# Kernel optimization log

Hardware: AMD Instinct MI355X
Metric: run time of the kernel (lower is better)

The kernel has to match this reference:

```python
import jax, jax.numpy as jnp
import numpy as np

N_QUBITS = 8
N_LAYERS = 2


def _apply_1q(state, U, wire, n):
    # state: (bs, 2**n); U: (2,2) fixed or (bs,2,2) batched; wire 0 = most significant
    bs = state.shape[0]
    left = 2 ** wire
    right = 2 ** (n - wire - 1)
    s = state.reshape(bs, left, 2, right)
    if U.ndim == 2:
        s = jnp.einsum('ij,bljr->blir', U, s)
    else:
        s = jnp.einsum('bij,bljr->blir', U, s)
    return s.reshape(bs, -1)


def _apply_ctrl(state, U, control, target, n):
    # apply 2x2 U on `target` where `control` qubit is |1>
    bs = state.shape[0]
    left = 2 ** control
    right = 2 ** (n - control - 1)
    s = state.reshape(bs, left, 2, right)
    s0 = s[:, :, 0, :].reshape(bs, -1)
    s1 = s[:, :, 1, :].reshape(bs, -1)
    t = target if target < control else target - 1  # target index among remaining n-1 wires
    s1 = _apply_1q(s1, U, t, n - 1)
    s = jnp.stack([s0.reshape(bs, left, right), s1.reshape(bs, left, right)], axis=2)
    return s.reshape(bs, -1)


def _rz_batched(theta):
    h = 0.5 * theta
    c, s = jnp.cos(h), jnp.sin(h)
    z = jnp.zeros_like(c)
    row0 = jnp.stack([c - 1j * s, z + 0j], axis=-1)
    row1 = jnp.stack([z + 0j, c + 1j * s], axis=-1)
    return jnp.stack([row0, row1], axis=-2).astype(jnp.complex64)  # (bs,2,2)


def _ry_batched(theta):
    h = 0.5 * theta
    c, s = jnp.cos(h), jnp.sin(h)
    row0 = jnp.stack([c, -s], axis=-1)
    row1 = jnp.stack([s, c], axis=-1)
    return jnp.stack([row0, row1], axis=-2).astype(jnp.complex64)


def _rx_fixed(theta):
    h = 0.5 * theta
    c, s = jnp.cos(h), jnp.sin(h)
    return jnp.stack([jnp.stack([c + 0j, -1j * s]), jnp.stack([-1j * s, c + 0j])]).astype(jnp.complex64)


def _ry_fixed(theta):
    h = 0.5 * theta
    c, s = jnp.cos(h), jnp.sin(h)
    return jnp.stack([jnp.stack([c + 0j, -s + 0j]), jnp.stack([s + 0j, c + 0j])]).astype(jnp.complex64)


def _circuit(X, weights):
    bs, L = X.shape
    n = N_QUBITS
    vpq = L // n + 1  # var_per_qubit
    state = jnp.zeros((bs, 2 ** n), jnp.complex64).at[:, 0].set(1.0)
    H = jnp.asarray(np.array([[1, 1], [1, -1]], np.complex64) / np.sqrt(2))
    # encoding: Hadamard then alternating RZ/RY per qubit
    for q in range(n):
        state = _apply_1q(state, H, q, n)
        for i in range(vpq):
            idx = q * vpq + i
            if idx >= L:
                break
            th = X[:, idx]
            U = _rz_batched(th) if i % 2 == 0 else _ry_batched(th)
            state = _apply_1q(state, U, q, n)
    # entangling ring: layer 0 -> CRX, layer 1 -> CRY ((l+1)%2==0 -> CRY)
    for l in range(N_LAYERS):
        for i in range(n):
            th = weights[l, i]
            U = _ry_fixed(th) if (l + 1) % 2 == 0 else _rx_fixed(th)
            state = _apply_ctrl(state, U, i, (i + 1) % n, n)
    # PauliZ expectation on each wire
    p = state.real ** 2 + state.imag ** 2  # (bs, 256)
    outs = []
    for q in range(n):
        pq = p.reshape(bs, 2 ** q, 2, -1).sum(axis=(1, 3))  # (bs, 2)
        outs.append(pq[:, 0] - pq[:, 1])
    return jnp.stack(outs, axis=1)  # (bs, 8)


def setup_inputs() -> dict:
    key = jax.random.key(0)
    k1, k2 = jax.random.split(key)
    X = jax.random.normal(k1, (16384, 64), dtype=jnp.float32)
    weights = jax.random.normal(k2, (N_LAYERS, N_LAYERS * N_QUBITS), dtype=jnp.float32)
    return {"X": X, "weights": weights}


def reference(X, weights):
    return _circuit(X, weights)
```

## Files before the change

kernel.cpp:

```cpp
#include <hip/hip_runtime.h>

#define DEV __device__ __forceinline__
typedef float f32x2 __attribute__((ext_vector_type(2)));
typedef float f32x4 __attribute__((ext_vector_type(4)));

DEV float rdlane(float v, int l) {
  return __int_as_float(__builtin_amdgcn_readlane(__float_as_int(v), l));
}
DEV f32x2 pkfma(f32x2 a, f32x2 b, f32x2 c) { return __builtin_elementwise_fma(a, b, c); }
DEV f32x2 splat(float x) { return (f32x2){x, x}; }
DEV f32x2 swap2(f32x2 v) { return __builtin_shufflevector(v, v, 1, 0); }
DEV f32x2 cmul(f32x2 P, f32x2 F) {
  f32x2 t = swap2(P);
  f32x2 m = {-t.x, t.y};
  return pkfma(splat(F.y), m, splat(F.x) * P);
}

template <int CTRL>
DEV float dppmov(float v) {
  return __int_as_float(__builtin_amdgcn_update_dpp(
      0, __float_as_int(v), CTRL, 0xf, 0xf, true));
}
template <int M>
DEV float xorl(float v) {
  if constexpr (M == 1)       return dppmov<0xB1>(v);
  else if constexpr (M == 2)  return dppmov<0x4E>(v);
  else if constexpr (M == 8)  return dppmov<0x128>(v);
  else if constexpr (M == 4)
    return __int_as_float(__builtin_amdgcn_ds_swizzle(__float_as_int(v), 0x101F));
  else
    return __int_as_float(__builtin_amdgcn_ds_swizzle(__float_as_int(v), 0x401F));
}

template <int M, bool CRX, int R0, int RS>
DEV void gate_lane(f32x2 amp[8], int lane, float c1, float s1) {
  const f32x2 C2 = splat(c1);
  if constexpr (CRX) {
    const f32x2 S2 = {s1, -s1};
#pragma unroll
    for (int r = R0; r < 8; r += RS) {
      f32x2 p;
      p.x = xorl<M>(amp[r].y);
      p.y = xorl<M>(amp[r].x);
      amp[r] = pkfma(S2, p, C2 * amp[r]);
    }
  } else {
    const float sp = (lane & M) ? s1 : -s1;
    const f32x2 SP = splat(sp);
#pragma unroll
    for (int r = R0; r < 8; r += RS) {
      f32x2 p;
      p.x = xorl<M>(amp[r].x);
      p.y = xorl<M>(amp[r].y);
      amp[r] = pkfma(SP, p, C2 * amp[r]);
    }
  }
}

template <bool CRX>
DEV void gate_pair(f32x2& aI, f32x2& aJ, float c1, float s1) {
  const f32x2 C2 = splat(c1);
  f32x2 nI, nJ;
  if constexpr (CRX) {
    const f32x2 S2 = {s1, -s1};
    nI = pkfma(S2, swap2(aJ), C2 * aI);
    nJ = pkfma(S2, swap2(aI), C2 * aJ);
  } else {
    nI = pkfma(splat(-s1), aJ, C2 * aI);
    nJ = pkfma(splat(s1), aI, C2 * aJ);
  }
  aI = nI; aJ = nJ;
}

__global__ __launch_bounds__(256, 4) void qsim_kernel(const float* __restrict__ X,
                                                      const float* __restrict__ W,
                                                      float* __restrict__ out, int bs) {
  const int lane = threadIdx.x & 63;
  const int wave = blockIdx.x * (blockDim.x >> 6) + (threadIdx.x >> 6);
  const int b0 = wave * 2;
  if (b0 >= bs) return;

  const float w = W[(((lane & 15) >> 3) << 4) + (lane & 7)];

  const int ce = (lane >> 3) & 1;
  const int cq = lane & 7;
  int bb = b0 + ce; bb = bb >= bs ? bs - 1 : bb;
  const float* Xrow = X + (size_t)bb * 64;
  const int lb = (cq == 7) ? 55 : cq * 9;
  f32x4 v0, v1;
  __builtin_memcpy(&v0, Xrow + lb, 16);
  __builtin_memcpy(&v1, Xrow + lb + 4, 16);
  const float a8 = Xrow[lb + 8];
  float ang[9] = {v0.x, v0.y, v0.z, v0.w, v1.x, v1.y, v1.z, v1.w, a8};
  if (cq == 7) ang[0] = a8;

  const float Hc = 0.70710678118654752440f;
  f32x2 A = {Hc, 0.f}, B = {Hc, 0.f};
#pragma unroll
  for (int i = 0; i < 9; ++i) {
    float s, c;
    __sincosf(0.5f * ang[i], &s, &c);
    if (i > 0) {
      bool dead = (cq == 7);
      c = dead ? 1.f : c;
      s = dead ? 0.f : s;
    }
    if ((i & 1) == 0) {
      f32x2 nA = pkfma((f32x2){s, -s}, swap2(A), splat(c) * A);
      f32x2 nB = pkfma((f32x2){-s, s}, swap2(B), splat(c) * B);
      A = nA; B = nB;
    } else {
      f32x2 nA = pkfma(splat(-s), B, splat(c) * A);
      f32x2 nB = pkfma(splat(c), B, splat(s) * A);
      A = nA; B = nB;
    }
  }

  __shared__ f32x4 ldsAB[4][16];
  const int wvid = (threadIdx.x >> 6) & 3;
  if (lane < 16) ldsAB[wvid][lane] = (f32x4){A.x, A.y, B.x, B.y};
  __builtin_amdgcn_wave_barrier();

  float sw, cw;
  __sincosf(0.5f * w, &sw, &cw);

  const int half = lane >> 5;
  const int base = half * 8;
  const f32x2* b2 = (const f32x2*)&ldsAB[wvid][0];
  f32x2 P = b2[(base + 0) * 2 + ((lane >> 4) & 1)];
#pragma unroll
  for (int q = 1; q <= 4; ++q)
    P = cmul(P, b2[(base + q) * 2 + ((lane >> (4 - q)) & 1)]);
  f32x4 F5 = ldsAB[wvid][base + 5];
  f32x4 F6 = ldsAB[wvid][base + 6];
  f32x4 F7 = ldsAB[wvid][base + 7];
  f32x2 A5 = {F5.x, F5.y}, B5 = {F5.z, F5.w};
  f32x2 A6 = {F6.x, F6.y}, B6 = {F6.z, F6.w};
  f32x2 A7 = {F7.x, F7.y}, B7 = {F7.z, F7.w};
  f32x2 amp[8];
  {
    f32x2 t0 = cmul(P, A5), t1 = cmul(P, B5);
    f32x2 u00 = cmul(t0, A6), u01 = cmul(t0, B6);
    amp[0] = cmul(u00, A7); amp[1] = cmul(u00, B7);
    amp[2] = cmul(u01, A7); amp[3] = cmul(u01, B7);
    f32x2 u10 = cmul(t1, A6), u11 = cmul(t1, B6);
    amp[4] = cmul(u10, A7); amp[5] = cmul(u10, B7);
    amp[6] = cmul(u11, A7); amp[7] = cmul(u11, B7);
  }

#pragma unroll
  for (int l = 0; l < 2; ++l) {
    const bool isCRX = (l == 0);
#define CS(G, CBIT) \
    const float cg = rdlane(cw, G), sg = rdlane(sw, G); \
    const bool act = (lane >> (CBIT)) & 1; \
    const float c1 = act ? cg : 1.f, s1 = act ? sg : 0.f;
    { CS(l * 8 + 0, 4)
      if (isCRX) gate_lane<8, true, 0, 1>(amp, lane, c1, s1);
      else       gate_lane<8, false, 0, 1>(amp, lane, c1, s1); }
    { CS(l * 8 + 1, 3)
      if (isCRX) gate_lane<4, true, 0, 1>(amp, lane, c1, s1);
      else       gate_lane<4, false, 0, 1>(amp, lane, c1, s1); }
    { CS(l * 8 + 2, 2)
      if (isCRX) gate_lane<2, true, 0, 1>(amp, lane, c1, s1);
      else       gate_lane<2, false, 0, 1>(amp, lane, c1, s1); }
    { CS(l * 8 + 3, 1)
      if (isCRX) gate_lane<1, true, 0, 1>(amp, lane, c1, s1);
      else       gate_lane<1, false, 0, 1>(amp, lane, c1, s1); }
    { CS(l * 8 + 4, 0)
#pragma unroll
      for (int r = 0; r < 4; ++r) {
        if (isCRX) gate_pair<true>(amp[r], amp[r + 4], c1, s1);
        else       gate_pair<false>(amp[r], amp[r + 4], c1, s1);
      } }
    {
      const float cg = rdlane(cw, l * 8 + 5), sg = rdlane(sw, l * 8 + 5);
      if (isCRX) { gate_pair<true>(amp[4], amp[6], cg, sg);
                   gate_pair<true>(amp[5], amp[7], cg, sg); }
      else       { gate_pair<false>(amp[4], amp[6], cg, sg);
                   gate_pair<false>(amp[5], amp[7], cg, sg); }
    }
    {
      const float cg = rdlane(cw, l * 8 + 6), sg = rdlane(sw, l * 8 + 6);
      if (isCRX) { gate_pair<true>(amp[2], amp[3], cg, sg);
                   gate_pair<true>(amp[6], amp[7], cg, sg); }
      else       { gate_pair<false>(amp[2], amp[3], cg, sg);
                   gate_pair<false>(amp[6], amp[7], cg, sg); }
    }
    {
      const float cg = rdlane(cw, l * 8 + 7), sg = rdlane(sw, l * 8 + 7);
      if (isCRX) gate_lane<16, true, 1, 2>(amp, lane, cg, sg);
      else       gate_lane<16, false, 1, 2>(amp, lane, cg, sg);
    }
#undef CS
  }

  float p[8];
#pragma unroll
  for (int r = 0; r < 8; ++r) p[r] = fmaf(amp[r].x, amp[r].x, amp[r].y * amp[r].y);
  float s01 = p[0] + p[1], s23 = p[2] + p[3], s45 = p[4] + p[5], s67 = p[6] + p[7];
  float sL = s01 + s23, sH = s45 + s67;
  float wv = sL + sH;
  f32x2 D = {sL - sH,
             (s01 + s45) - (s23 + s67)};
  float d7 = (p[0] - p[1]) + (p[2] - p[3]) + (p[4] - p[5]) + (p[6] - p[7]);

#define STAGE(K, M)                                   \
  {                                                   \
    float pp = xorl<M>(wv);                           \
    wv = pp + (((lane >> K) & 1) ? -wv : wv);         \
    f32x2 pd;                                         \
    pd.x = xorl<M>(D.x);                              \
    pd.y = xorl<M>(D.y);                              \
    D = D + pd;                                       \
    d7 += xorl<M>(d7);                                \
  }
  STAGE(0, 1) STAGE(1, 2) STAGE(2, 4) STAGE(3, 8) STAGE(4, 16)
#undef STAGE

  const int lpos = lane & 31;
  const int srcl = (lane & 32) + (16 >> lpos);
  float g = __shfl(wv, srcl, 64);
  float val = (lpos == 5) ? D.x : (lpos == 6) ? D.y : (lpos == 7) ? d7 : g;
  const int brow = b0 + half;
  if (lpos < 8 && brow < bs) out[(size_t)brow * 8 + lpos] = val;
}

extern "C" void kernel_launch(void* const* d_in, const int* in_sizes, int n_in,
                              void* d_out, int out_size, void* d_ws, size_t ws_size,
                              hipStream_t stream) {
  const float* X = (const float*)d_in[0];
  const float* W = (const float*)d_in[1];
  float* out = (float*)d_out;
  int bs = in_sizes[0] / 64;
  int waves = (bs + 1) / 2;
  const int waves_per_block = 4;
  const int threads = waves_per_block * 64;
  int blocks = (waves + waves_per_block - 1) / waves_per_block;
  hipLaunchKernelGGL(qsim_kernel, dim3(blocks), dim3(threads), 0, stream, X, W, out, bs);
}
```

Baseline: 64.10 us.

## Pack four batch samples per wave with 16 amplitudes per lane

Each wave now simulates four circuits instead of two, so each lane holds 16 amplitudes, and 16 lanes cover one 256-amplitude state. The qubit-to-lane mapping is redone: more gates become in-register pair updates, fewer need cross-lane DPP or swizzle, and the Z-expectation reduction needs one fewer shuffle stage. This halves the wave count and cuts cross-lane traffic per sample. The cost is higher register pressure from 16 complex amplitudes per lane, which could reduce occupancy under the 256x4 launch bounds.

```diff
diff --git a/kernel.cpp b/kernel.cpp
--- a/kernel.cpp
+++ b/kernel.cpp
@@ -26,19 +26,17 @@
   if constexpr (M == 1)       return dppmov<0xB1>(v);
   else if constexpr (M == 2)  return dppmov<0x4E>(v);
   else if constexpr (M == 8)  return dppmov<0x128>(v);
-  else if constexpr (M == 4)
+  else
     return __int_as_float(__builtin_amdgcn_ds_swizzle(__float_as_int(v), 0x101F));
-  else
-    return __int_as_float(__builtin_amdgcn_ds_swizzle(__float_as_int(v), 0x401F));
 }
 
 template <int M, bool CRX, int R0, int RS>
-DEV void gate_lane(f32x2 amp[8], int lane, float c1, float s1) {
+DEV void gate_lane16(f32x2 amp[16], int lane, float c1, float s1) {
   const f32x2 C2 = splat(c1);
   if constexpr (CRX) {
     const f32x2 S2 = {s1, -s1};
 #pragma unroll
-    for (int r = R0; r < 8; r += RS) {
+    for (int r = R0; r < 16; r += RS) {
       f32x2 p;
       p.x = xorl<M>(amp[r].y);
       p.y = xorl<M>(amp[r].x);
@@ -48,7 +46,7 @@
     const float sp = (lane & M) ? s1 : -s1;
     const f32x2 SP = splat(sp);
 #pragma unroll
-    for (int r = R0; r < 8; r += RS) {
+    for (int r = R0; r < 16; r += RS) {
       f32x2 p;
       p.x = xorl<M>(amp[r].x);
       p.y = xorl<M>(amp[r].y);
@@ -77,13 +75,14 @@
                                                       float* __restrict__ out, int bs) {
   const int lane = threadIdx.x & 63;
   const int wave = blockIdx.x * (blockDim.x >> 6) + (threadIdx.x >> 6);
-  const int b0 = wave * 2;
+  const int b0 = wave * 4;
   if (b0 >= bs) return;
 
   const float w = W[(((lane & 15) >> 3) << 4) + (lane & 7)];
 
-  const int ce = (lane >> 3) & 1;
-  const int cq = lane & 7;
+  const int cidx = lane & 31;
+  const int ce = cidx >> 3;
+  const int cq = cidx & 7;
   int bb = b0 + ce; bb = bb >= bs ? bs - 1 : bb;
   const float* Xrow = X + (size_t)bb * 64;
   const int lb = (cq == 7) ? 55 : cq * 9;
@@ -116,36 +115,44 @@
     }
   }
 
-  __shared__ f32x4 ldsAB[4][16];
+  __shared__ f32x4 ldsAB[4][32];
   const int wvid = (threadIdx.x >> 6) & 3;
-  if (lane < 16) ldsAB[wvid][lane] = (f32x4){A.x, A.y, B.x, B.y};
+  if (lane < 32) ldsAB[wvid][cidx] = (f32x4){A.x, A.y, B.x, B.y};
   __builtin_amdgcn_wave_barrier();
 
   float sw, cw;
   __sincosf(0.5f * w, &sw, &cw);
 
-  const int half = lane >> 5;
-  const int base = half * 8;
+  const int grp = lane >> 4;
+  const int cbase = grp * 8;
   const f32x2* b2 = (const f32x2*)&ldsAB[wvid][0];
-  f32x2 P = b2[(base + 0) * 2 + ((lane >> 4) & 1)];
-#pragma unroll
-  for (int q = 1; q <= 4; ++q)
-    P = cmul(P, b2[(base + q) * 2 + ((lane >> (4 - q)) & 1)]);
-  f32x4 F5 = ldsAB[wvid][base + 5];
-  f32x4 F6 = ldsAB[wvid][base + 6];
-  f32x4 F7 = ldsAB[wvid][base + 7];
+  f32x2 P = b2[(cbase + 0) * 2 + ((lane >> 3) & 1)];
+#pragma unroll
+  for (int q = 1; q <= 3; ++q)
+    P = cmul(P, b2[(cbase + q) * 2 + ((lane >> (3 - q)) & 1)]);
+  f32x4 F4 = ldsAB[wvid][cbase + 4];
+  f32x4 F5 = ldsAB[wvid][cbase + 5];
+  f32x4 F6 = ldsAB[wvid][cbase + 6];
+  f32x4 F7 = ldsAB[wvid][cbase + 7];
+  f32x2 A4 = {F4.x, F4.y}, B4 = {F4.z, F4.w};
   f32x2 A5 = {F5.x, F5.y}, B5 = {F5.z, F5.w};
   f32x2 A6 = {F6.x, F6.y}, B6 = {F6.z, F6.w};
   f32x2 A7 = {F7.x, F7.y}, B7 = {F7.z, F7.w};
-  f32x2 amp[8];
+  f32x2 amp[16];
   {
-    f32x2 t0 = cmul(P, A5), t1 = cmul(P, B5);
-    f32x2 u00 = cmul(t0, A6), u01 = cmul(t0, B6);
-    amp[0] = cmul(u00, A7); amp[1] = cmul(u00, B7);
-    amp[2] = cmul(u01, A7); amp[3] = cmul(u01, B7);
-    f32x2 u10 = cmul(t1, A6), u11 = cmul(t1, B6);
-    amp[4] = cmul(u10, A7); amp[5] = cmul(u10, B7);
-    amp[6] = cmul(u11, A7); amp[7] = cmul(u11, B7);
+    f32x2 t0 = cmul(P, A4);
+    f32x2 u00 = cmul(t0, A5), u01 = cmul(t0, B5);
+    f32x2 v;
+    v = cmul(u00, A6); amp[0] = cmul(v, A7);  amp[1] = cmul(v, B7);
+    v = cmul(u00, B6); amp[2] = cmul(v, A7);  amp[3] = cmul(v, B7);
+    v = cmul(u01, A6); amp[4] = cmul(v, A7);  amp[5] = cmul(v, B7);
+    v = cmul(u01, B6); amp[6] = cmul(v, A7);  amp[7] = cmul(v, B7);
+    f32x2 t1 = cmul(P, B4);
+    f32x2 u10 = cmul(t1, A5), u11 = cmul(t1, B5);
+    v = cmul(u10, A6); amp[8] = cmul(v, A7);  amp[9] = cmul(v, B7);
+    v = cmul(u10, B6); amp[10] = cmul(v, A7); amp[11] = cmul(v, B7);
+    v = cmul(u11, A6); amp[12] = cmul(v, A7); amp[13] = cmul(v, B7);
+    v = cmul(u11, B6); amp[14] = cmul(v, A7); amp[15] = cmul(v, B7);
   }
 
 #pragma unroll
@@ -155,74 +162,95 @@
     const float cg = rdlane(cw, G), sg = rdlane(sw, G); \
     const bool act = (lane >> (CBIT)) & 1; \
     const float c1 = act ? cg : 1.f, s1 = act ? sg : 0.f;
-    { CS(l * 8 + 0, 4)
-      if (isCRX) gate_lane<8, true, 0, 1>(amp, lane, c1, s1);
-      else       gate_lane<8, false, 0, 1>(amp, lane, c1, s1); }
-    { CS(l * 8 + 1, 3)
-      if (isCRX) gate_lane<4, true, 0, 1>(amp, lane, c1, s1);
-      else       gate_lane<4, false, 0, 1>(amp, lane, c1, s1); }
-    { CS(l * 8 + 2, 2)
-      if (isCRX) gate_lane<2, true, 0, 1>(amp, lane, c1, s1);
-      else       gate_lane<2, false, 0, 1>(amp, lane, c1, s1); }
-    { CS(l * 8 + 3, 1)
-      if (isCRX) gate_lane<1, true, 0, 1>(amp, lane, c1, s1);
-      else       gate_lane<1, false, 0, 1>(amp, lane, c1, s1); }
-    { CS(l * 8 + 4, 0)
-#pragma unroll
-      for (int r = 0; r < 4; ++r) {
-        if (isCRX) gate_pair<true>(amp[r], amp[r + 4], c1, s1);
-        else       gate_pair<false>(amp[r], amp[r + 4], c1, s1);
+    { CS(l * 8 + 0, 3)
+      if (isCRX) gate_lane16<4, true, 0, 1>(amp, lane, c1, s1);
+      else       gate_lane16<4, false, 0, 1>(amp, lane, c1, s1); }
+    { CS(l * 8 + 1, 2)
+      if (isCRX) gate_lane16<2, true, 0, 1>(amp, lane, c1, s1);
+      else       gate_lane16<2, false, 0, 1>(amp, lane, c1, s1); }
+    { CS(l * 8 + 2, 1)
+      if (isCRX) gate_lane16<1, true, 0, 1>(amp, lane, c1, s1);
+      else       gate_lane16<1, false, 0, 1>(amp, lane, c1, s1); }
+    { CS(l * 8 + 3, 0)
+#pragma unroll
+      for (int r = 0; r < 8; ++r) {
+        if (isCRX) gate_pair<true>(amp[r], amp[r + 8], c1, s1);
+        else       gate_pair<false>(amp[r], amp[r + 8], c1, s1);
       } }
+    {
+      const float cg = rdlane(cw, l * 8 + 4), sg = rdlane(sw, l * 8 + 4);
+#pragma unroll
+      for (int r = 8; r < 12; ++r) {
+        if (isCRX) gate_pair<true>(amp[r], amp[r + 4], cg, sg);
+        else       gate_pair<false>(amp[r], amp[r + 4], cg, sg);
+      }
+    }
     {
       const float cg = rdlane(cw, l * 8 + 5), sg = rdlane(sw, l * 8 + 5);
       if (isCRX) { gate_pair<true>(amp[4], amp[6], cg, sg);
-                   gate_pair<true>(amp[5], amp[7], cg, sg); }
+                   gate_pair<true>(amp[5], amp[7], cg, sg);
+                   gate_pair<true>(amp[12], amp[14], cg, sg);
+                   gate_pair<true>(amp[13], amp[15], cg, sg); }
       else       { gate_pair<false>(amp[4], amp[6], cg, sg);
-                   gate_pair<false>(amp[5], amp[7], cg, sg); }
+                   gate_pair<false>(amp[5], amp[7], cg, sg);
+                   gate_pair<false>(amp[12], amp[14], cg, sg);
+                   gate_pair<false>(amp[13], amp[15], cg, sg); }
     }
     {
       const float cg = rdlane(cw, l * 8 + 6), sg = rdlane(sw, l * 8 + 6);
       if (isCRX) { gate_pair<true>(amp[2], amp[3], cg, sg);
-                   gate_pair<true>(amp[6], amp[7], cg, sg); }
+                   gate_pair<true>(amp[6], amp[7], cg, sg);
+                   gate_pair<true>(amp[10], amp[11], cg, sg);
+                   gate_pair<true>(amp[14], amp[15], cg, sg); }
       else       { gate_pair<false>(amp[2], amp[3], cg, sg);
-                   gate_pair<false>(amp[6], amp[7], cg, sg); }
+                   gate_pair<false>(amp[6], amp[7], cg, sg);
+                   gate_pair<false>(amp[10], amp[11], cg, sg);
+                   gate_pair<false>(amp[14], amp[15], cg, sg); }
     }
     {
       const float cg = rdlane(cw, l * 8 + 7), sg = rdlane(sw, l * 8 + 7);
-      if (isCRX) gate_lane<16, true, 1, 2>(amp, lane, cg, sg);
-      else       gate_lane<16, false, 1, 2>(amp, lane, cg, sg);
+      if (isCRX) gate_lane16<8, true, 1, 2>(amp, lane, cg, sg);
+      else       gate_lane16<8, false, 1, 2>(amp, lane, cg, sg);
     }
 #undef CS
   }
 
-  float p[8];
-#pragma unroll
-  for (int r = 0; r < 8; ++r) p[r] = fmaf(amp[r].x, amp[r].x, amp[r].y * amp[r].y);
-  float s01 = p[0] + p[1], s23 = p[2] + p[3], s45 = p[4] + p[5], s67 = p[6] + p[7];
-  float sL = s01 + s23, sH = s45 + s67;
-  float wv = sL + sH;
-  f32x2 D = {sL - sH,
-             (s01 + s45) - (s23 + s67)};
-  float d7 = (p[0] - p[1]) + (p[2] - p[3]) + (p[4] - p[5]) + (p[6] - p[7]);
-
-#define STAGE(K, M)                                   \
+  float p[16];
+#pragma unroll
+  for (int r = 0; r < 16; ++r) p[r] = fmaf(amp[r].x, amp[r].x, amp[r].y * amp[r].y);
+  float s2[8], d2[8];
+#pragma unroll
+  for (int k = 0; k < 8; ++k) { s2[k] = p[2 * k] + p[2 * k + 1]; d2[k] = p[2 * k] - p[2 * k + 1]; }
+  float d7 = ((d2[0] + d2[1]) + (d2[2] + d2[3])) + ((d2[4] + d2[5]) + (d2[6] + d2[7]));
+  float s4[4], e4[4];
+#pragma unroll
+  for (int k = 0; k < 4; ++k) { s4[k] = s2[2 * k] + s2[2 * k + 1]; e4[k] = s2[2 * k] - s2[2 * k + 1]; }
+  float d6 = (e4[0] + e4[1]) + (e4[2] + e4[3]);
+  float s8a = s4[0] + s4[1], s8b = s4[2] + s4[3];
+  float d5 = (s4[0] - s4[1]) + (s4[2] - s4[3]);
+  float S = s8a + s8b;
+  float d4 = s8a - s8b;
+  f32x2 D45 = {d4, d5}, D67 = {d6, d7};
+
+#define STG(K, M)                                     \
   {                                                   \
-    float pp = xorl<M>(wv);                           \
-    wv = pp + (((lane >> K) & 1) ? -wv : wv);         \
-    f32x2 pd;                                         \
-    pd.x = xorl<M>(D.x);                              \
-    pd.y = xorl<M>(D.y);                              \
-    D = D + pd;                                       \
-    d7 += xorl<M>(d7);                                \
-  }
-  STAGE(0, 1) STAGE(1, 2) STAGE(2, 4) STAGE(3, 8) STAGE(4, 16)
-#undef STAGE
-
-  const int lpos = lane & 31;
-  const int srcl = (lane & 32) + (16 >> lpos);
-  float g = __shfl(wv, srcl, 64);
-  float val = (lpos == 5) ? D.x : (lpos == 6) ? D.y : (lpos == 7) ? d7 : g;
-  const int brow = b0 + half;
+    float pp = xorl<M>(S);                            \
+    S = pp + (((lane >> K) & 1) ? -S : S);            \
+    f32x2 qa, qb;                                     \
+    qa.x = xorl<M>(D45.x); qa.y = xorl<M>(D45.y);     \
+    D45 = D45 + qa;                                   \
+    qb.x = xorl<M>(D67.x); qb.y = xorl<M>(D67.y);     \
+    D67 = D67 + qb;                                   \
+  }
+  STG(0, 1) STG(1, 2) STG(2, 4) STG(3, 8)
+#undef STG
+
+  const int lpos = lane & 15;
+  const int srcl = (lane & 48) + (8 >> lpos);
+  float g = __shfl(S, srcl, 64);
+  float val = (lpos == 4) ? D45.x : (lpos == 5) ? D45.y
+            : (lpos == 6) ? D67.x : (lpos == 7) ? D67.y : g;
+  const int brow = b0 + (lane >> 4);
   if (lpos < 8 && brow < bs) out[(size_t)brow * 8 + lpos] = val;
 }
 
@@ -233,7 +261,7 @@
   const float* W = (const float*)d_in[1];
   float* out = (float*)d_out;
   int bs = in_sizes[0] / 64;
-  int waves = (bs + 1) / 2;
+  int waves = (bs + 3) / 4;
   const int waves_per_block = 4;
   const int threads = waves_per_block * 64;
   int blocks = (waves + waves_per_block - 1) / waves_per_block;
```

Result: faster. 62.32 us (-2.8%).
